# Optimization experiments

Hardware: AMD Instinct MI355X
Metric: run time of the kernel (lower is better)

## Reference

```python
import jax, jax.numpy as jnp
import numpy as np

W = 128        # word_size
N_LOC = 16384  # n_locations
B = 64
D_CTRL = 1024
EPS_NORM = 1e-12   # F.normalize eps
EPS_SHARP = 1e-9


def setup_inputs() -> dict:
    key = jax.random.key(0)
    k1, k2, k3, k4, k5 = jax.random.split(key, 5)
    controller_state = jax.random.normal(k1, (B, D_CTRL), dtype=jnp.float32)
    memory = jax.random.uniform(k2, (N_LOC, W), dtype=jnp.float32)
    w_prev = jax.random.uniform(k3, (B, N_LOC), dtype=jnp.float32)
    w_prev = w_prev / jnp.sum(w_prev, axis=-1, keepdims=True)  # valid attention dist
    total_out = 3 * W + 6  # key(W)+beta(1)+gate(1)+shift(3)+gamma(1)+erase(W)+add(W)
    fc_w = jax.random.normal(k4, (total_out, D_CTRL), dtype=jnp.float32) * (1.0 / np.sqrt(D_CTRL))
    fc_b = jax.random.normal(k5, (total_out,), dtype=jnp.float32) * 0.01
    return {"controller_state": controller_state, "memory": memory,
            "w_prev": w_prev, "fc_w": fc_w, "fc_b": fc_b}


def _l2_normalize(x, axis=-1):
    n = jnp.sqrt(jnp.sum(x * x, axis=axis, keepdims=True))
    return x / jnp.maximum(n, EPS_NORM)


def reference(controller_state, memory, w_prev, fc_w, fc_b):
    raw = controller_state @ fc_w.T + fc_b  # [B, 3W+6]
    key = raw[:, :W]
    beta = jax.nn.softplus(raw[:, W:W + 1])
    gate = jax.nn.sigmoid(raw[:, W + 1:W + 2])
    shift = jax.nn.softmax(raw[:, W + 2:W + 5], axis=-1)
    gamma = jax.nn.softplus(raw[:, W + 5:W + 6]) + 1.0
    erase = jax.nn.sigmoid(raw[:, W + 6:2 * W + 6])
    add = jnp.tanh(raw[:, 2 * W + 6:3 * W + 6])

    # content addressing: cosine sim + softmax(beta * sim)
    sim = _l2_normalize(key) @ _l2_normalize(memory).T  # [B, N_LOC]
    w_content = jax.nn.softmax(beta * sim, axis=-1)

    # location addressing
    w_g = gate * w_content + (1.0 - gate) * w_prev
    w_shifted = (shift[:, 0:1] * jnp.roll(w_g, 1, axis=1)
                 + shift[:, 1:2] * w_g
                 + shift[:, 2:3] * jnp.roll(w_g, -1, axis=1))
    w_pow = jnp.clip(w_shifted, EPS_SHARP, None) ** gamma
    w_new = w_pow / (jnp.sum(w_pow, axis=-1, keepdims=True) + EPS_SHARP)

    # write: mean over batch of outer products w_new[b] x erase/add[b]
    # == (w_new^T @ erase) / B  (same math as bmm(...).mean(0), no [B,N,W] temp)
    inv_b = 1.0 / w_new.shape[0]
    erase_mean = jnp.einsum('bn,bw->nw', w_new, erase) * inv_b
    add_mean = jnp.einsum('bn,bw->nw', w_new, add) * inv_b
    new_memory = memory * (1.0 - erase_mean) + add_mean
    return w_new, new_memory
```

## Files before the change

kernel.cpp:

```cpp
#include <hip/hip_runtime.h>
#include <math.h>

#define N_LOC 16384
#define W 128
#define B_SZ 64
#define TOTAL_OUT 390

__device__ __forceinline__ float dot4(float4 a, float4 b) {
    return a.x * b.x + a.y * b.y + a.z * b.z + a.w * b.w;
}
__device__ __forceinline__ float softplus_f(float x) {
    return fmaxf(x, 0.0f) + log1pf(expf(-fabsf(x)));
}
__device__ __forceinline__ float sigmoid_f(float x) {
    return 1.0f / (1.0f + expf(-x));
}
__device__ __forceinline__ float wave_reduce_sum(float v) {
#pragma unroll
    for (int off = 32; off >= 1; off >>= 1) v += __shfl_xor(v, off);
    return v;
}

__global__ __launch_bounds__(256) void kA(const float* __restrict__ cs,
                                          const float* __restrict__ fcw,
                                          const float* __restrict__ fcb,
                                          float* __restrict__ raw) {
    __shared__ float4 cs4[8][256];
    const int t = threadIdx.x;
    const int blk = blockIdx.x;
    const int oc = blk % 98;
    const int btile = blk / 98;

    const float4* csg = reinterpret_cast<const float4*>(cs);
#pragma unroll
    for (int i = 0; i < 8; i++) {
        int f4 = t + 256 * i;
        int row = f4 >> 8;
        int col = f4 & 255;
        cs4[row][col] = csg[(btile * 8 + row) * 256 + col];
    }
    __syncthreads();

    const int lane = t & 63;
    const int wv = t >> 6;
    const int o = oc * 4 + wv;
    if (o >= TOTAL_OUT) return;

    const float4* fcw4 = reinterpret_cast<const float4*>(fcw);
    float4 r0 = fcw4[o * 256 + 0 * 64 + lane];
    float4 r1 = fcw4[o * 256 + 1 * 64 + lane];
    float4 r2 = fcw4[o * 256 + 2 * 64 + lane];
    float4 r3 = fcw4[o * 256 + 3 * 64 + lane];
    const float bias = fcb[o];
#pragma unroll
    for (int b = 0; b < 8; b++) {
        float acc = dot4(cs4[b][0 * 64 + lane], r0);
        acc += dot4(cs4[b][1 * 64 + lane], r1);
        acc += dot4(cs4[b][2 * 64 + lane], r2);
        acc += dot4(cs4[b][3 * 64 + lane], r3);
        acc = wave_reduce_sum(acc);
        if (lane == 0) {
            raw[(btile * 8 + b) * TOTAL_OUT + o] = acc + bias;
        }
    }
}

__global__ __launch_bounds__(256) void kB(const float* __restrict__ mem,
                                          const float* __restrict__ raw,
                                          float* __restrict__ e_buf,
                                          float* __restrict__ partialS) {
    __shared__ float4 kb4[B_SZ][32];
    __shared__ float betaS[B_SZ];
    const int t = threadIdx.x;
    const int blk = blockIdx.x;

    {
        const int b = t >> 2;
        const int q = t & 3;
        const float* rb = raw + b * TOTAL_OUT;
        const float2* rk = reinterpret_cast<const float2*>(rb) + q * 16;
        float2 v[16];
        float ss = 0.0f;
#pragma unroll
        for (int j = 0; j < 16; j++) {
            v[j] = rk[j];
            ss += v[j].x * v[j].x + v[j].y * v[j].y;
        }
        ss += __shfl_xor(ss, 1);
        ss += __shfl_xor(ss, 2);
        const float beta = softplus_f(rb[W]);
        const float scale = beta / fmaxf(sqrtf(ss), 1e-12f);
        if (q == 0) betaS[b] = beta;
#pragma unroll
        for (int jj = 0; jj < 8; jj++) {
            kb4[b][q * 8 + jj] = make_float4(v[2 * jj].x * scale,
                                             v[2 * jj].y * scale,
                                             v[2 * jj + 1].x * scale,
                                             v[2 * jj + 1].y * scale);
        }
    }
    __syncthreads();

    const int nl = t & 15;
    const int bg = t >> 4;
    const int n = blk * 16 + nl;
    const float4* mrow = reinterpret_cast<const float4*>(mem) + (size_t)n * 32;

    float acc[4];
#pragma unroll
    for (int i = 0; i < 4; i++) acc[i] = 0.0f;
    float nrm = 0.0f;
#pragma unroll 8
    for (int k4 = 0; k4 < 32; k4++) {
        float4 mv = mrow[k4];
        nrm += dot4(mv, mv);
#pragma unroll
        for (int bi = 0; bi < 4; bi++)
            acc[bi] += dot4(kb4[bg * 4 + bi][k4], mv);
    }
    const float r = 1.0f / fmaxf(sqrtf(nrm), 1e-12f);
    float ev[4];
#pragma unroll
    for (int bi = 0; bi < 4; bi++) {
        const int b = bg * 4 + bi;
        float e = __expf(acc[bi] * r - betaS[b]);
        ev[bi] = e;
        e_buf[(size_t)b * N_LOC + n] = e;
    }
#pragma unroll
    for (int bi = 0; bi < 4; bi++) {
        float v = ev[bi];
        v += __shfl_xor(v, 1);
        v += __shfl_xor(v, 2);
        v += __shfl_xor(v, 4);
        v += __shfl_xor(v, 8);
        ev[bi] = v;
    }
    if (nl == 0) {
#pragma unroll
        for (int bi = 0; bi < 4; bi++)
            partialS[(size_t)(bg * 4 + bi) * 1024 + blk] = ev[bi];
    }
}

__global__ __launch_bounds__(256) void kC(const float* __restrict__ e_buf,
                                          const float* __restrict__ wprev,
                                          const float* __restrict__ raw,
                                          const float* __restrict__ partialS,
                                          float* __restrict__ p_buf,
                                          float* __restrict__ partialP,
                                          float* __restrict__ erase,
                                          float* __restrict__ addv) {
    __shared__ float rC[4];
    __shared__ float cpar[5];
    const int t = threadIdx.x;
    const int blk = blockIdx.x;
    const int b = blk >> 3, c = blk & 7;
    const float* rb = raw + b * TOTAL_OUT;

    const float* ps = partialS + (size_t)b * 1024;
    float sv = ps[t] + ps[t + 256] + ps[t + 512] + ps[t + 768];
    sv = wave_reduce_sum(sv);
    if ((t & 63) == 0) rC[t >> 6] = sv;
    if (t == 0) {
        cpar[0] = sigmoid_f(rb[W + 1]);
        cpar[1] = softplus_f(rb[W + 5]) + 1.0f;
        float s0 = rb[W + 2], s1 = rb[W + 3], s2 = rb[W + 4];
        float m = fmaxf(s0, fmaxf(s1, s2));
        float e0 = expf(s0 - m), e1 = expf(s1 - m), e2 = expf(s2 - m);
        float si = 1.0f / (e0 + e1 + e2);
        cpar[2] = e0 * si;
        cpar[3] = e1 * si;
        cpar[4] = e2 * si;
    }
    __syncthreads();
    const float S = rC[0] + rC[1] + rC[2] + rC[3];

    const float gate = cpar[0];
    const float ga = gate / S;
    const float og = 1.0f - gate;
    const float gm = cpar[1];
    const float sh0 = cpar[2];
    const float sh1 = cpar[3];
    const float sh2 = cpar[4];

    if (c == 0) {
        if (t < 128) erase[b * W + t] = sigmoid_f(rb[W + 6 + t]);
        else         addv[b * W + (t - 128)] = tanhf(rb[2 * W + 6 + (t - 128)]);
    }

    const float* erow = e_buf + (size_t)b * N_LOC;
    const float* wrow = wprev + (size_t)b * N_LOC;
    const int nb = c * 2048 + 8 * t;

    float4 e0v = *reinterpret_cast<const float4*>(erow + nb);
    float4 e1v = *reinterpret_cast<const float4*>(erow + nb + 4);
    float4 w0 = *reinterpret_cast<const float4*>(wrow + nb);
    float4 w1 = *reinterpret_cast<const float4*>(wrow + nb + 4);
    const int nm1 = (nb + N_LOC - 1) & (N_LOC - 1);
    const int np8 = (nb + 8) & (N_LOC - 1);

    float g[10];
    g[0] = ga * erow[nm1] + og * wrow[nm1];
    g[1] = ga * e0v.x + og * w0.x;
    g[2] = ga * e0v.y + og * w0.y;
    g[3] = ga * e0v.z + og * w0.z;
    g[4] = ga * e0v.w + og * w0.w;
    g[5] = ga * e1v.x + og * w1.x;
    g[6] = ga * e1v.y + og * w1.y;
    g[7] = ga * e1v.z + og * w1.z;
    g[8] = ga * e1v.w + og * w1.w;
    g[9] = ga * erow[np8] + og * wrow[np8];

    float p[8];
    float sp = 0.0f;
#pragma unroll
    for (int j = 0; j < 8; j++) {
        float x = fmaxf(sh0 * g[j] + sh1 * g[j + 1] + sh2 * g[j + 2], 1e-9f);
        p[j] = exp2f(gm * __log2f(x));
        sp += p[j];
    }
    *reinterpret_cast<float4*>(p_buf + (size_t)b * N_LOC + nb) =
        make_float4(p[0], p[1], p[2], p[3]);
    *reinterpret_cast<float4*>(p_buf + (size_t)b * N_LOC + nb + 4) =
        make_float4(p[4], p[5], p[6], p[7]);

    sp = wave_reduce_sum(sp);
    __syncthreads();
    if ((t & 63) == 0) rC[t >> 6] = sp;
    __syncthreads();
    if (t == 0) partialP[b * 8 + c] = rC[0] + rC[1] + rC[2] + rC[3];
}

__global__ __launch_bounds__(256) void kD(const float* __restrict__ mem,
                                          const float* __restrict__ erase,
                                          const float* __restrict__ addv,
                                          const float* __restrict__ partialP,
                                          float* __restrict__ p_buf,
                                          float* __restrict__ outmem) {
    __shared__ float invb[B_SZ];
    const int t = threadIdx.x;
    const int blk = blockIdx.x;
    if (t < B_SZ) {
        const float* pp = partialP + t * 8;
        float s = 0.0f;
#pragma unroll
        for (int j = 0; j < 8; j++) s += pp[j];
        invb[t] = 1.0f / (s + 1e-9f);
    }
    __syncthreads();

    const int w = t & 127;
    const int nh = t >> 7;
    const int nb = blk * 32;
    const int nbase = nb + nh * 16;

    float ae[16], aa[16];
#pragma unroll
    for (int i = 0; i < 16; i++) { ae[i] = 0.0f; aa[i] = 0.0f; }

    for (int b = 0; b < B_SZ; b++) {
        const float ib = invb[b] * (1.0f / 64.0f);
        const float wei = erase[b * W + w] * ib;
        const float wai = addv[b * W + w] * ib;
        const float4* pr4 =
            reinterpret_cast<const float4*>(p_buf + (size_t)b * N_LOC + nbase);
#pragma unroll
        for (int i4 = 0; i4 < 4; i4++) {
            float4 v = pr4[i4];
            ae[i4 * 4 + 0] += v.x * wei; aa[i4 * 4 + 0] += v.x * wai;
            ae[i4 * 4 + 1] += v.y * wei; aa[i4 * 4 + 1] += v.y * wai;
            ae[i4 * 4 + 2] += v.z * wei; aa[i4 * 4 + 2] += v.z * wai;
            ae[i4 * 4 + 3] += v.w * wei; aa[i4 * 4 + 3] += v.w * wai;
        }
    }
#pragma unroll
    for (int i = 0; i < 16; i++) {
        const int n = nbase + i;
        float mv = mem[(size_t)n * W + w];
        outmem[(size_t)n * W + w] = mv * (1.0f - ae[i]) + aa[i];
    }
    __syncthreads();
    const int b8 = t >> 5, nl = t & 31;
#pragma unroll
    for (int bi = 0; bi < 8; bi++) {
        const int b = bi * 8 + b8;
        const size_t idx = (size_t)b * N_LOC + nb + nl;
        p_buf[idx] *= invb[b];
    }
}

extern "C" void kernel_launch(void* const* d_in, const int* in_sizes, int n_in,
                              void* d_out, int out_size, void* d_ws, size_t ws_size,
                              hipStream_t stream) {
    const float* cs    = (const float*)d_in[0];
    const float* mem   = (const float*)d_in[1];
    const float* wprev = (const float*)d_in[2];
    const float* fcw   = (const float*)d_in[3];
    const float* fcb   = (const float*)d_in[4];

    float* out = (float*)d_out;
    float* p_buf = out;
    float* emem = out + (size_t)B_SZ * N_LOC;

    float* wsf = (float*)d_ws;
    float* raw      = wsf;
    float* erase    = raw + 24960;
    float* addv     = erase + 8192;
    float* partialS = addv + 8192;
    float* partialP = partialS + 65536;

    kA<<<784, 256, 0, stream>>>(cs, fcw, fcb, raw);
    kB<<<1024, 256, 0, stream>>>(mem, raw, emem, partialS);
    kC<<<512, 256, 0, stream>>>(emem, wprev, raw, partialS, p_buf, partialP,
                                erase, addv);
    kD<<<512, 256, 0, stream>>>(mem, erase, addv, partialP, p_buf, emem);
}
```

Before: 66.95 us.

## Read controller state from global in kA; stage erase/add in LDS in kD

kA no longer stages the 8-row controller-state tile in shared memory. Each wave now reads its float4 slices straight from global memory, which drops the LDS fill and the barrier but means every wave re-reads the same rows and relies on the cache. kD preloads the full erase and add matrices (64x128 each, 64 KB total) into shared memory and unrolls the batch loop by 4, replacing scattered global loads inside the hot loop. The larger LDS footprint in kD may lower occupancy.

```diff
diff --git a/kernel.cpp b/kernel.cpp
--- a/kernel.cpp
+++ b/kernel.cpp
@@ -25,28 +25,18 @@
                                           const float* __restrict__ fcw,
                                           const float* __restrict__ fcb,
                                           float* __restrict__ raw) {
-    __shared__ float4 cs4[8][256];
     const int t = threadIdx.x;
     const int blk = blockIdx.x;
     const int oc = blk % 98;
     const int btile = blk / 98;
 
-    const float4* csg = reinterpret_cast<const float4*>(cs);
-#pragma unroll
-    for (int i = 0; i < 8; i++) {
-        int f4 = t + 256 * i;
-        int row = f4 >> 8;
-        int col = f4 & 255;
-        cs4[row][col] = csg[(btile * 8 + row) * 256 + col];
-    }
-    __syncthreads();
-
     const int lane = t & 63;
     const int wv = t >> 6;
     const int o = oc * 4 + wv;
     if (o >= TOTAL_OUT) return;
 
     const float4* fcw4 = reinterpret_cast<const float4*>(fcw);
+    const float4* csg = reinterpret_cast<const float4*>(cs);
     float4 r0 = fcw4[o * 256 + 0 * 64 + lane];
     float4 r1 = fcw4[o * 256 + 1 * 64 + lane];
     float4 r2 = fcw4[o * 256 + 2 * 64 + lane];
@@ -54,10 +44,11 @@
     const float bias = fcb[o];
 #pragma unroll
     for (int b = 0; b < 8; b++) {
-        float acc = dot4(cs4[b][0 * 64 + lane], r0);
-        acc += dot4(cs4[b][1 * 64 + lane], r1);
-        acc += dot4(cs4[b][2 * 64 + lane], r2);
-        acc += dot4(cs4[b][3 * 64 + lane], r3);
+        const float4* cb = csg + (btile * 8 + b) * 256;
+        float acc = dot4(cb[0 * 64 + lane], r0);
+        acc += dot4(cb[1 * 64 + lane], r1);
+        acc += dot4(cb[2 * 64 + lane], r2);
+        acc += dot4(cb[3 * 64 + lane], r3);
         acc = wave_reduce_sum(acc);
         if (lane == 0) {
             raw[(btile * 8 + b) * TOTAL_OUT + o] = acc + bias;
@@ -239,6 +230,8 @@
                                           float* __restrict__ p_buf,
                                           float* __restrict__ outmem) {
     __shared__ float invb[B_SZ];
+    __shared__ float eL[B_SZ][W];
+    __shared__ float aL[B_SZ][W];
     const int t = threadIdx.x;
     const int blk = blockIdx.x;
     if (t < B_SZ) {
@@ -248,6 +241,17 @@
         for (int j = 0; j < 8; j++) s += pp[j];
         invb[t] = 1.0f / (s + 1e-9f);
     }
+    {
+        const float4* eg = reinterpret_cast<const float4*>(erase);
+        const float4* ag = reinterpret_cast<const float4*>(addv);
+        float4* el4 = reinterpret_cast<float4*>(&eL[0][0]);
+        float4* al4 = reinterpret_cast<float4*>(&aL[0][0]);
+#pragma unroll
+        for (int i = 0; i < 8; i++) {
+            el4[t + 256 * i] = eg[t + 256 * i];
+            al4[t + 256 * i] = ag[t + 256 * i];
+        }
+    }
     __syncthreads();
 
     const int w = t & 127;
@@ -259,10 +263,11 @@
 #pragma unroll
     for (int i = 0; i < 16; i++) { ae[i] = 0.0f; aa[i] = 0.0f; }
 
+#pragma unroll 4
     for (int b = 0; b < B_SZ; b++) {
         const float ib = invb[b] * (1.0f / 64.0f);
-        const float wei = erase[b * W + w] * ib;
-        const float wai = addv[b * W + w] * ib;
+        const float wei = eL[b][w] * ib;
+        const float wai = aL[b][w] * ib;
         const float4* pr4 =
             reinterpret_cast<const float4*>(p_buf + (size_t)b * N_LOC + nbase);
 #pragma unroll
```

Result: faster. 59.99 us (-10.4%).
